# Optimization experiments

Hardware: AMD Instinct MI355X
Metric: run time of the kernel (lower is better)

## Reference

```python
import jax, jax.numpy as jnp
import numpy as np

N, M, C = 4096, 1024, 64
KERNEL_SIZE = (0.1, 0.1)  # box extents; threshold is kernel_size/2 on |dx|,|dy|


def setup_inputs() -> dict:
    key = jax.random.key(0)
    k1, k2, k3 = jax.random.split(key, 3)
    values = jax.random.normal(k1, (N, C), dtype=jnp.float32)
    coords = jax.random.uniform(k2, (N, 2), dtype=jnp.float32)
    query_coords = jax.random.uniform(k3, (M, 2), dtype=jnp.float32)
    return {"values": values, "coords": coords, "query_coords": query_coords}


def reference(values, coords, query_coords):
    # shift buffer is (0,0) so no shift branch; box-kernel mask branch.
    kw, kh = KERNEL_SIZE
    diffs = query_coords[:, None, :] - coords[None, :, :]          # [M, N, 2]
    mask = (jnp.abs(diffs[..., 0]) < kw / 2) & (jnp.abs(diffs[..., 1]) < kh / 2)  # [M, N]
    neg = jnp.finfo(values.dtype).min
    # per-query masked max over points == ragged split + per-segment max in the original
    masked = jnp.where(mask[:, :, None], values[None, :, :], neg)  # [M, N, C]
    return jnp.max(masked, axis=1)                                  # [M, C]
```

## Files before the change

### kernel.cpp

```cpp
#include <hip/hip_runtime.h>

constexpr int N = 4096;
constexpr int M = 1024;
constexpr int C = 64;
#define HALF_KW 0.05f
#define NEG_INF (-3.402823466e38f)

__global__ __launch_bounds__(256) void maxpool_box_kernel(
    const float* __restrict__ values,
    const float* __restrict__ coords,
    const float* __restrict__ qcoords,
    float* __restrict__ out)
{
    __shared__ int    s_cnt;
    __shared__ int    s_list[N];
    __shared__ float4 s_part[16][16];

    const int q    = blockIdx.x;
    const int tid  = threadIdx.x;
    const int lane = tid & 63;
    const int w    = tid >> 6;

    if (tid == 0) s_cnt = 0;
    __syncthreads();

    const float qx = qcoords[2 * q + 0];
    const float qy = qcoords[2 * q + 1];

    const float4* c4p = (const float4*)coords;
    #pragma unroll
    for (int i = 0; i < N / (256 * 2); ++i) {
        const int pair = i * 256 + tid;
        const float4 cc = c4p[pair];
        const bool in0 = (fabsf(qx - cc.x) < HALF_KW) && (fabsf(qy - cc.y) < HALF_KW);
        const bool in1 = (fabsf(qx - cc.z) < HALF_KW) && (fabsf(qy - cc.w) < HALF_KW);
        if (in0) { int k = atomicAdd(&s_cnt, 1); s_list[k] = 2 * pair; }
        if (in1) { int k = atomicAdd(&s_cnt, 1); s_list[k] = 2 * pair + 1; }
    }
    __syncthreads();

    const int cnt = s_cnt;
    const int G   = (cnt + 3) >> 2;
    if (cnt > 0 && tid < G * 4 - cnt) s_list[cnt + tid] = s_list[0];
    __syncthreads();

    const int sub = lane >> 4;
    const int cq  = lane & 15;
    const float4* v4 = (const float4*)values;
    float4 acc = make_float4(NEG_INF, NEG_INF, NEG_INF, NEG_INF);
    for (int g = w; g < G; g += 4) {
        const int p = s_list[g * 4 + sub];
        const float4 v = v4[p * 16 + cq];
        acc.x = fmaxf(acc.x, v.x);
        acc.y = fmaxf(acc.y, v.y);
        acc.z = fmaxf(acc.z, v.z);
        acc.w = fmaxf(acc.w, v.w);
    }
    s_part[w * 4 + sub][cq] = acc;
    __syncthreads();

    if (tid < 16) {
        float4 r = s_part[0][tid];
        #pragma unroll
        for (int k = 1; k < 16; ++k) {
            const float4 t = s_part[k][tid];
            r.x = fmaxf(r.x, t.x);
            r.y = fmaxf(r.y, t.y);
            r.z = fmaxf(r.z, t.z);
            r.w = fmaxf(r.w, t.w);
        }
        ((float4*)out)[q * 16 + tid] = r;
    }
}

extern "C" void kernel_launch(void* const* d_in, const int* in_sizes, int n_in,
                              void* d_out, int out_size, void* d_ws, size_t ws_size,
                              hipStream_t stream) {
    const float* values  = (const float*)d_in[0];
    const float* coords  = (const float*)d_in[1];
    const float* qcoords = (const float*)d_in[2];
    float* out = (float*)d_out;

    maxpool_box_kernel<<<M, 256, 0, stream>>>(values, coords, qcoords, out);
}
```

Measured before the change: 61.80 us.

## Use per-wave ballot compaction and wave-local lists instead of shared atomics

```diff
diff --git a/kernel.cpp b/kernel.cpp
--- a/kernel.cpp
+++ b/kernel.cpp
@@ -12,57 +12,66 @@
     const float* __restrict__ qcoords,
     float* __restrict__ out)
 {
-    __shared__ int    s_cnt;
     __shared__ int    s_list[N];
-    __shared__ float4 s_part[16][16];
+    __shared__ float4 s_part[4][16];
 
-    const int q    = blockIdx.x;
     const int tid  = threadIdx.x;
     const int lane = tid & 63;
     const int w    = tid >> 6;
-
-    if (tid == 0) s_cnt = 0;
-    __syncthreads();
+    const int q    = blockIdx.x;
 
     const float qx = qcoords[2 * q + 0];
     const float qy = qcoords[2 * q + 1];
 
-    const float4* c4p = (const float4*)coords;
+    const int wbase = w << 10;
+    int wcnt = 0;
+    const float4* c4 = (const float4*)coords;
+    const unsigned long long lt = (1ULL << lane) - 1;
+
     #pragma unroll
-    for (int i = 0; i < N / (256 * 2); ++i) {
-        const int pair = i * 256 + tid;
-        const float4 cc = c4p[pair];
+    for (int i = 0; i < 8; ++i) {
+        const int pair = (w << 9) + (i << 6) + lane;
+        const float4 cc = c4[pair];
         const bool in0 = (fabsf(qx - cc.x) < HALF_KW) && (fabsf(qy - cc.y) < HALF_KW);
         const bool in1 = (fabsf(qx - cc.z) < HALF_KW) && (fabsf(qy - cc.w) < HALF_KW);
-        if (in0) { int k = atomicAdd(&s_cnt, 1); s_list[k] = 2 * pair; }
-        if (in1) { int k = atomicAdd(&s_cnt, 1); s_list[k] = 2 * pair + 1; }
+        const unsigned long long m0 = __ballot(in0);
+        const unsigned long long m1 = __ballot(in1);
+        const int c0 = __popcll(m0);
+        if (in0) s_list[wbase + wcnt + __popcll(m0 & lt)]      = 2 * pair;
+        if (in1) s_list[wbase + wcnt + c0 + __popcll(m1 & lt)] = 2 * pair + 1;
+        wcnt += c0 + __popcll(m1);
     }
-    __syncthreads();
-
-    const int cnt = s_cnt;
-    const int G   = (cnt + 3) >> 2;
-    if (cnt > 0 && tid < G * 4 - cnt) s_list[cnt + tid] = s_list[0];
-    __syncthreads();
 
     const int sub = lane >> 4;
     const int cq  = lane & 15;
     const float4* v4 = (const float4*)values;
     float4 acc = make_float4(NEG_INF, NEG_INF, NEG_INF, NEG_INF);
-    for (int g = w; g < G; g += 4) {
-        const int p = s_list[g * 4 + sub];
+    const int G = (wcnt + 3) >> 2;
+    for (int g = 0; g < G; ++g) {
+        int ii = (g << 2) + sub;
+        ii = ii < wcnt ? ii : 0;
+        const int p = s_list[wbase + ii];
         const float4 v = v4[p * 16 + cq];
         acc.x = fmaxf(acc.x, v.x);
         acc.y = fmaxf(acc.y, v.y);
         acc.z = fmaxf(acc.z, v.z);
         acc.w = fmaxf(acc.w, v.w);
     }
-    s_part[w * 4 + sub][cq] = acc;
+
+    #pragma unroll
+    for (int d = 16; d < 64; d <<= 1) {
+        acc.x = fmaxf(acc.x, __shfl_xor(acc.x, d, 64));
+        acc.y = fmaxf(acc.y, __shfl_xor(acc.y, d, 64));
+        acc.z = fmaxf(acc.z, __shfl_xor(acc.z, d, 64));
+        acc.w = fmaxf(acc.w, __shfl_xor(acc.w, d, 64));
+    }
+    if (lane < 16) s_part[w][cq] = acc;
     __syncthreads();
 
     if (tid < 16) {
         float4 r = s_part[0][tid];
         #pragma unroll
-        for (int k = 1; k < 16; ++k) {
+        for (int k = 1; k < 4; ++k) {
             const float4 t = s_part[k][tid];
             r.x = fmaxf(r.x, t.x);
             r.y = fmaxf(r.y, t.y);
```

After: 62.00 us. Within noise of the previous version (+0.3%).
